# Kernel optimization log

Measured on AMD Instinct MI355X. Metric: run time of the kernel, lower is better.

The kernel has to match this reference:

```python
import jax, jax.numpy as jnp
import numpy as np
import math

B, D, TX, TY = 16, 192, 512, 2048
NEG = -1e9


def _neg_cent(x_mean, x_logs, z):
    # x_mean, x_logs: [B, D, TX]; z: [B, D, TY] -> neg_cent: [B, TY, TX]
    s_p_sq_r = jnp.exp(-2.0 * x_logs)                                   # [B,D,TX]
    nc1 = jnp.sum(-0.5 * math.log(2.0 * math.pi) - x_logs, axis=1, keepdims=True)  # [B,1,TX]
    nc2 = jnp.einsum('bdy,bdx->byx', -0.5 * z * z, s_p_sq_r)            # [B,TY,TX]
    nc3 = jnp.einsum('bdy,bdx->byx', z, x_mean * s_p_sq_r)              # [B,TY,TX]
    nc4 = jnp.sum(-0.5 * x_mean * x_mean * s_p_sq_r, axis=1, keepdims=True)  # [B,1,TX]
    return nc1 + nc2 + nc3 + nc4


def _mas_single(nc):
    # Monotonic alignment search (Viterbi DP) for one sample. nc: [TY, TX]
    ty, tx = nc.shape
    xs = jnp.arange(tx)

    def fwd_step(v_prev, inp):
        nc_row, y = inp
        v_diag = jnp.concatenate([jnp.full((1,), NEG, nc.dtype), v_prev[:-1]])
        take_diag = v_diag > v_prev                                      # bool [TX]
        v = nc_row + jnp.maximum(v_prev, v_diag)
        v = jnp.where(xs <= y, v, NEG)                                   # path cannot be ahead of time
        return v, take_diag

    v0 = jnp.where(xs == 0, nc[0], NEG)
    _, dirs = jax.lax.scan(fwd_step, v0, (nc[1:], jnp.arange(1, ty)))    # dirs: [TY-1, TX]

    def bwd_step(idx, d_row):
        # idx = path position at row y; move to y-1
        new_idx = idx - d_row[idx].astype(idx.dtype)
        return new_idx, idx

    idx0, path_tail = jax.lax.scan(bwd_step, jnp.array(tx - 1, jnp.int32), dirs, reverse=True)
    path = jnp.concatenate([idx0[None], path_tail])                      # [TY]
    return jax.nn.one_hot(path, tx, dtype=nc.dtype)                      # [TY, TX]


def _forward(x_mean, x_logs, z, logw):
    neg_cent = jax.lax.stop_gradient(_neg_cent(x_mean, x_logs, z))
    attn = jax.lax.stop_gradient(jax.vmap(_mas_single)(neg_cent))        # [B,TY,TX]
    w = jnp.sum(attn, axis=1, keepdims=True)                             # [B,1,TX] durations
    logw_ = jnp.log(w + 1e-6)
    l_length = jnp.sum((logw - logw_) ** 2, axis=(1, 2))                 # [B]
    m_p = jnp.einsum('byx,bdx->bdy', attn, x_mean)                       # [B,D,TY]
    logs_p = jnp.einsum('byx,bdx->bdy', attn, x_logs)                    # [B,D,TY]
    out_main = jnp.concatenate([m_p, logs_p], axis=1)                    # [B,2D,TY]
    return out_main, l_length, attn


def setup_inputs() -> dict:
    key = jax.random.key(0)
    k1, k2, k3, k4 = jax.random.split(key, 4)
    return {
        'x_mean': jax.random.normal(k1, (B, D, TX), jnp.float32),
        'x_logs': jax.random.normal(k2, (B, D, TX), jnp.float32),
        'z': jax.random.normal(k3, (B, D, TY), jnp.float32),
        'logw': jax.random.normal(k4, (B, 1, TX), jnp.float32),
    }


def reference(x_mean, x_logs, z, logw):
    return _forward(x_mean, x_logs, z, logw)
```

## Files before the change

kernel.cpp:

```cpp
#include <hip/hip_runtime.h>
#include <hip/hip_bf16.h>
#include <math.h>

#define B_   16
#define D_   192
#define TX_  512
#define TY_  2048
#define NEGV (-1e9f)



typedef __attribute__((address_space(1))) const float glob_f;
typedef __attribute__((address_space(3))) float       lds_f;

__global__ __launch_bounds__(512) void precomp(const float* __restrict__ xm,
                                               const float* __restrict__ xl,
                                               float* __restrict__ S,
                                               float* __restrict__ MS,
                                               float* __restrict__ Cpart) {
    int b = blockIdx.x;
    int p = blockIdx.y;
    int x = threadIdx.x;
    size_t base = ((size_t)b * D_ + p * 32) * TX_;
    const float* mb = xm + base;
    const float* lb = xl + base;
    float* Sb  = S  + base;
    float* MSb = MS + base;
    float c = 0.f;
    for (int d = 0; d < 32; d++) {
        float lg = lb[d * TX_ + x];
        float mn = mb[d * TX_ + x];
        float s  = expf(-2.f * lg);
        float ms = mn * s;
        Sb[d * TX_ + x]  = s;
        MSb[d * TX_ + x] = ms;
        c += -0.9189385332046727f - lg - 0.5f * mn * mn * s;
    }
    Cpart[(b * 6 + p) * TX_ + x] = c;
}

__global__ __launch_bounds__(256) void gemm_nc(const float* __restrict__ z,
                                               const float* __restrict__ S,
                                               const float* __restrict__ MS,
                                               const float* __restrict__ Cpart,
                                               float* __restrict__ NC) {
    int bx = blockIdx.x;
    int by = blockIdx.y;
    int b  = blockIdx.z;
    int tid = threadIdx.x;
    int tx = tid & 15, ty = tid >> 4;
    __shared__ __align__(16) float Zt[16 * 128];
    __shared__ __align__(16) float St[16 * 128];
    __shared__ __align__(16) float MSt[16 * 128];

    float acc[8][8];
#pragma unroll
    for (int i = 0; i < 8; i++)
#pragma unroll
        for (int j = 0; j < 8; j++) acc[i][j] = 0.f;

    int x0 = bx * 128, y0 = by * 128;
    const float* zb  = z  + (size_t)b * D_ * TY_;
    const float* Sb  = S  + (size_t)b * D_ * TX_;
    const float* MSb = MS + (size_t)b * D_ * TX_;

    for (int k0 = 0; k0 < D_; k0 += 16) {
#pragma unroll
        for (int j = 0; j < 2; j++) {
            int f = tid + j * 256;
            int kk = f >> 5, c = (f & 31) * 4;
            __builtin_amdgcn_global_load_lds((glob_f*)(zb  + (size_t)(k0 + kk) * TY_ + y0 + c),
                                             (lds_f*)(Zt  + f * 4), 16, 0, 0);
            __builtin_amdgcn_global_load_lds((glob_f*)(Sb  + (size_t)(k0 + kk) * TX_ + x0 + c),
                                             (lds_f*)(St  + f * 4), 16, 0, 0);
            __builtin_amdgcn_global_load_lds((glob_f*)(MSb + (size_t)(k0 + kk) * TX_ + x0 + c),
                                             (lds_f*)(MSt + f * 4), 16, 0, 0);
        }
        __syncthreads();

#pragma unroll 2
        for (int kk = 0; kk < 16; kk++) {
            float4 z0 = *(const float4*)&Zt[kk * 128 + ty * 4];
            float4 z1 = *(const float4*)&Zt[kk * 128 + 64 + ty * 4];
            float4 s0 = *(const float4*)&St[kk * 128 + tx * 4];
            float4 s1 = *(const float4*)&St[kk * 128 + 64 + tx * 4];
            float4 m0 = *(const float4*)&MSt[kk * 128 + tx * 4];
            float4 m1 = *(const float4*)&MSt[kk * 128 + 64 + tx * 4];
            float4 u0, u1;
            u0.x = -0.5f * z0.x * z0.x; u0.y = -0.5f * z0.y * z0.y;
            u0.z = -0.5f * z0.z * z0.z; u0.w = -0.5f * z0.w * z0.w;
            u1.x = -0.5f * z1.x * z1.x; u1.y = -0.5f * z1.y * z1.y;
            u1.z = -0.5f * z1.z * z1.z; u1.w = -0.5f * z1.w * z1.w;
            float zz[8] = {z0.x, z0.y, z0.z, z0.w, z1.x, z1.y, z1.z, z1.w};
            float uu[8] = {u0.x, u0.y, u0.z, u0.w, u1.x, u1.y, u1.z, u1.w};
            float ss[8] = {s0.x, s0.y, s0.z, s0.w, s1.x, s1.y, s1.z, s1.w};
            float mm[8] = {m0.x, m0.y, m0.z, m0.w, m1.x, m1.y, m1.z, m1.w};
#pragma unroll
            for (int i = 0; i < 8; i++)
#pragma unroll
                for (int j = 0; j < 8; j++)
                    acc[i][j] += uu[i] * ss[j] + zz[i] * mm[j];
        }
        __syncthreads();
    }

    float cv[8] = {0, 0, 0, 0, 0, 0, 0, 0};
#pragma unroll
    for (int p = 0; p < 6; p++) {
        float4 c0 = *(const float4*)&Cpart[(b * 6 + p) * TX_ + x0 + tx * 4];
        float4 c1 = *(const float4*)&Cpart[(b * 6 + p) * TX_ + x0 + 64 + tx * 4];
        cv[0] += c0.x; cv[1] += c0.y; cv[2] += c0.z; cv[3] += c0.w;
        cv[4] += c1.x; cv[5] += c1.y; cv[6] += c1.z; cv[7] += c1.w;
    }

#pragma unroll
    for (int i = 0; i < 8; i++) {
        int y = y0 + ty * 4 + (i & 3) + 64 * (i >> 2);
        float4 o0, o1;
        o0.x = acc[i][0] + cv[0]; o0.y = acc[i][1] + cv[1];
        o0.z = acc[i][2] + cv[2]; o0.w = acc[i][3] + cv[3];
        o1.x = acc[i][4] + cv[4]; o1.y = acc[i][5] + cv[5];
        o1.z = acc[i][6] + cv[6]; o1.w = acc[i][7] + cv[7];
        *(float4*)&NC[((size_t)b * TY_ + y) * TX_ + x0 + tx * 4]      = o0;
        *(float4*)&NC[((size_t)b * TY_ + y) * TX_ + x0 + 64 + tx * 4] = o1;
    }
}

__global__ __launch_bounds__(64, 1) void mas_forward(const float* __restrict__ NC,
                                                     unsigned char* __restrict__ dirs) {
    int b = blockIdx.x;
    int lane = threadIdx.x;
    const float* ncb = NC + (size_t)b * TY_ * TX_;
    const float4* base = (const float4*)ncb + lane * 2;

    float4 A[16], C[16];
#pragma unroll
    for (int s = 0; s < 16; s++) {
        A[s] = base[(size_t)(1 + s) * 128];
        C[s] = base[(size_t)(1 + s) * 128 + 1];
    }

    float v[8];
#pragma unroll
    for (int j = 0; j < 8; j++) v[j] = NEGV;
    if (lane == 0) v[0] = ncb[0];

    unsigned char* db = dirs + (size_t)b * 2048 * 64 + lane;

    float bound = NEGV;

    auto row_step = [&](float4 a, float4 c, int y, bool mask) {
        float ncv[8] = {a.x, a.y, a.z, a.w, c.x, c.y, c.z, c.w};
        float vd0 = (lane == 0) ? NEGV : bound;
        float v6o = v[6], v7o = v[7];
        float v7n = ncv[7] + fmaxf(v7o, v6o);
        if (mask && y < 511 && lane * 8 + 7 > y) v7n = NEGV;
        bound = __shfl_up(v7n, 1);
        unsigned bits = (v6o > v7o) ? 0x80u : 0u;
        float vd = vd0;
#pragma unroll
        for (int j = 0; j < 7; j++) {
            float vp = v[j];
            bits |= (vd > vp) ? (1u << j) : 0u;
            v[j] = ncv[j] + fmaxf(vp, vd);
            vd = vp;
        }
        if (mask && y < 511) {
            int xb = lane * 8;
#pragma unroll
            for (int j = 0; j < 7; j++)
                if (xb + j > y) v[j] = NEGV;
        }
        v[7] = v7n;
        db[(size_t)(y - 1) * 64] = (unsigned char)bits;
    };

    int y = 1;
    for (int k = 0; k < 32; k++) {
#pragma unroll
        for (int s = 0; s < 16; s++) {
            float4 a = A[s], c = C[s];
            A[s] = base[(size_t)(y + 16) * 128];
            C[s] = base[(size_t)(y + 16) * 128 + 1];
            row_step(a, c, y, true);
            y++;
        }
    }
    for (int k = 32; k < 127; k++) {
#pragma unroll
        for (int s = 0; s < 16; s++) {
            float4 a = A[s], c = C[s];
            A[s] = base[(size_t)(y + 16) * 128];
            C[s] = base[(size_t)(y + 16) * 128 + 1];
            row_step(a, c, y, false);
            y++;
        }
    }
#pragma unroll
    for (int s = 0; s < 15; s++) {
        row_step(A[s], C[s], y, false);
        y++;
    }
}

__global__ __launch_bounds__(64, 1) void mas_backtrack(const unsigned* __restrict__ dirs,
                                                       int* __restrict__ path) {
    int b = blockIdx.x;
    int lane = threadIdx.x;
    const unsigned* db = dirs + (size_t)b * 2048 * 16;
    int idx = TX_ - 1;

    for (int y_hi = 2047; y_hi >= 1; y_hi -= 64) {
        int wb = (idx >> 5) - 2;
        if (wb < 0) wb = 0;
        int base = wb << 5;
        int y = y_hi - lane;
        unsigned w0 = 0, w1 = 0, w2 = 0;
        if (y >= 1) {
            const unsigned* r = db + (size_t)(y - 1) * 16 + wb;
            w0 = r[0]; w1 = r[1]; w2 = r[2];
        }
        int steps = (y_hi < 64) ? y_hi : 64;
        int my_path = 0;
#pragma unroll 8
        for (int t = 0; t < steps; t++) {
            if (lane == t) my_path = idx;
            unsigned u0 = (unsigned)__shfl((int)w0, t);
            unsigned u1 = (unsigned)__shfl((int)w1, t);
            unsigned u2 = (unsigned)__shfl((int)w2, t);
            int off = idx - base;
            unsigned w = (off < 32) ? u0 : ((off < 64) ? u1 : u2);
            idx -= (int)((w >> (off & 31)) & 1u);
        }
        if (lane < steps) path[b * TY_ + (y_hi - lane)] = my_path;
    }
    if (lane == 0) path[b * TY_ + 0] = idx;
}

__global__ __launch_bounds__(512) void durations_ll(const int* __restrict__ path,
                                                    const float* __restrict__ logw,
                                                    float* __restrict__ out_l) {
    int b = blockIdx.x;
    int tid = threadIdx.x;
    __shared__ int wcnt[TX_];
    __shared__ float partial[8];
    wcnt[tid] = 0;
    __syncthreads();
    for (int y = tid; y < TY_; y += 512)
        atomicAdd(&wcnt[path[b * TY_ + y]], 1);
    __syncthreads();
    float t = logw[b * TX_ + tid] - logf((float)wcnt[tid] + 1e-6f);
    float sq = t * t;
#pragma unroll
    for (int off = 32; off > 0; off >>= 1) sq += __shfl_down(sq, off);
    if ((tid & 63) == 0) partial[tid >> 6] = sq;
    __syncthreads();
    if (tid == 0) {
        float s = 0.f;
#pragma unroll
        for (int i = 0; i < 8; i++) s += partial[i];
        out_l[b] = s;
    }
}

__global__ __launch_bounds__(256) void gather_main(const int* __restrict__ path,
                                                   const float* __restrict__ xm,
                                                   const float* __restrict__ xl,
                                                   float* __restrict__ out) {
    int c = blockIdx.x;
    int b = blockIdx.y;
    int tid = threadIdx.x;
    const float* src = (c < D_) ? (xm + ((size_t)b * D_ + c) * TX_)
                                : (xl + ((size_t)b * D_ + (c - D_)) * TX_);
    const int* pb = path + b * TY_;
    float* ob = out + ((size_t)b * 2 * D_ + c) * TY_;
#pragma unroll
    for (int k = 0; k < 8; k++) {
        int y = tid + k * 256;
        ob[y] = src[pb[y]];
    }
}

__global__ __launch_bounds__(128) void write_attn(const int* __restrict__ path,
                                                  float* __restrict__ attn) {
    int blk = blockIdx.x;
    int b = blk >> 11;
    int y = blk & 2047;
    int tid = threadIdx.x;
    int p = path[b * TY_ + y];
    float4 val = make_float4(0.f, 0.f, 0.f, 0.f);
    if ((p >> 2) == tid) {
        int r = p & 3;
        if (r == 0) val.x = 1.f;
        else if (r == 1) val.y = 1.f;
        else if (r == 2) val.z = 1.f;
        else val.w = 1.f;
    }
    ((float4*)attn)[((size_t)blk) * 128 + tid] = val;
}

extern "C" void kernel_launch(void* const* d_in, const int* in_sizes, int n_in,
                              void* d_out, int out_size, void* d_ws, size_t ws_size,
                              hipStream_t stream) {
    const float* x_mean = (const float*)d_in[0];
    const float* x_logs = (const float*)d_in[1];
    const float* z      = (const float*)d_in[2];
    const float* logw   = (const float*)d_in[3];
    float* out = (float*)d_out;

    char* ws = (char*)d_ws;
    float* S            = (float*)(ws + 0);
    float* MS           = (float*)(ws + 6291456);
    float* NC           = (float*)(ws + 12615680);
    unsigned char* dirs = (unsigned char*)(ws + 79724544);
    float* Cpart        = (float*)(ws + 79724544);
    int* path           = (int*)(ws + 81821696);

    float* out_main = out;
    float* out_l    = out + 12582912;
    float* out_attn = out + 12582928;

    precomp<<<dim3(B_, 6), dim3(512), 0, stream>>>(x_mean, x_logs, S, MS, Cpart);
    gemm_nc<<<dim3(4, 16, 16), dim3(256), 0, stream>>>(z, S, MS, Cpart, NC);
    mas_forward<<<dim3(B_), dim3(64), 0, stream>>>(NC, dirs);
    mas_backtrack<<<dim3(B_), dim3(64), 0, stream>>>((const unsigned*)dirs, path);
    durations_ll<<<dim3(B_), dim3(512), 0, stream>>>(path, logw, out_l);
    gather_main<<<dim3(384, 16), dim3(256), 0, stream>>>(path, x_mean, x_logs, out_main);
    write_attn<<<dim3(B_ * TY_), dim3(128), 0, stream>>>(path, out_attn);
}
```

Baseline: 752.3 us.

## Add producer wave streaming NC rows into LDS ring for MAS forward

The MAS forward kernel becomes a two-wave block: one producer wave copies chunks of 16 rows of neg_cent straight from global memory into a 4-slot LDS ring with global_load_lds, and the consumer wave runs the Viterbi recurrence from LDS. The two waves synchronise through workgroup-scope atomic counters with sleep-based spinning. This replaces the register-held 16-row prefetch, aiming to hide global load latency on the serial DP path. In exchange it adds 128KB of LDS, spin-wait overhead, and LDS read latency on every row.

```diff
diff --git a/kernel.cpp b/kernel.cpp
--- a/kernel.cpp
+++ b/kernel.cpp
@@ -126,80 +126,123 @@
     }
 }
 
-__global__ __launch_bounds__(64, 1) void mas_forward(const float* __restrict__ NC,
-                                                     unsigned char* __restrict__ dirs) {
+__global__ __launch_bounds__(128, 1) void mas_forward(const float* __restrict__ NC,
+                                                      unsigned char* __restrict__ dirs) {
     int b = blockIdx.x;
-    int lane = threadIdx.x;
+    int tid = threadIdx.x;
+    int wave = tid >> 6;
+    int lane = tid & 63;
     const float* ncb = NC + (size_t)b * TY_ * TX_;
-    const float4* base = (const float4*)ncb + lane * 2;
-
-    float4 A[16], C[16];
-#pragma unroll
-    for (int s = 0; s < 16; s++) {
-        A[s] = base[(size_t)(1 + s) * 128];
-        C[s] = base[(size_t)(1 + s) * 128 + 1];
-    }
-
-    float v[8];
-#pragma unroll
-    for (int j = 0; j < 8; j++) v[j] = NEGV;
-    if (lane == 0) v[0] = ncb[0];
-
-    unsigned char* db = dirs + (size_t)b * 2048 * 64 + lane;
-
-    float bound = NEGV;
-
-    auto row_step = [&](float4 a, float4 c, int y, bool mask) {
-        float ncv[8] = {a.x, a.y, a.z, a.w, c.x, c.y, c.z, c.w};
-        float vd0 = (lane == 0) ? NEGV : bound;
-        float v6o = v[6], v7o = v[7];
-        float v7n = ncv[7] + fmaxf(v7o, v6o);
-        if (mask && y < 511 && lane * 8 + 7 > y) v7n = NEGV;
-        bound = __shfl_up(v7n, 1);
-        unsigned bits = (v6o > v7o) ? 0x80u : 0u;
-        float vd = vd0;
-#pragma unroll
-        for (int j = 0; j < 7; j++) {
-            float vp = v[j];
-            bits |= (vd > vp) ? (1u << j) : 0u;
-            v[j] = ncv[j] + fmaxf(vp, vd);
-            vd = vp;
-        }
-        if (mask && y < 511) {
-            int xb = lane * 8;
-#pragma unroll
-            for (int j = 0; j < 7; j++)
-                if (xb + j > y) v[j] = NEGV;
-        }
-        v[7] = v7n;
-        db[(size_t)(y - 1) * 64] = (unsigned char)bits;
-    };
-
-    int y = 1;
-    for (int k = 0; k < 32; k++) {
-#pragma unroll
-        for (int s = 0; s < 16; s++) {
-            float4 a = A[s], c = C[s];
-            A[s] = base[(size_t)(y + 16) * 128];
-            C[s] = base[(size_t)(y + 16) * 128 + 1];
-            row_step(a, c, y, true);
-            y++;
-        }
-    }
-    for (int k = 32; k < 127; k++) {
-#pragma unroll
-        for (int s = 0; s < 16; s++) {
-            float4 a = A[s], c = C[s];
-            A[s] = base[(size_t)(y + 16) * 128];
-            C[s] = base[(size_t)(y + 16) * 128 + 1];
-            row_step(a, c, y, false);
-            y++;
-        }
-    }
-#pragma unroll
-    for (int s = 0; s < 15; s++) {
-        row_step(A[s], C[s], y, false);
-        y++;
+
+    __shared__ __align__(16) float ring[64][512];
+    __shared__ int prod_cnt;
+    __shared__ int cons_cnt;
+    if (tid == 0) { prod_cnt = 0; cons_cnt = 0; }
+    __syncthreads();
+
+    if (wave == 1) {
+        for (int k = 0; k < 128; k++) {
+            while (k - __hip_atomic_load(&cons_cnt, __ATOMIC_ACQUIRE,
+                                         __HIP_MEMORY_SCOPE_WORKGROUP) >= 4)
+                __builtin_amdgcn_s_sleep(1);
+            int slot0 = (k & 3) * 16;
+#pragma unroll
+            for (int r = 0; r < 16; r++) {
+                int y = 1 + k * 16 + r;
+                if (y > 2047) y = 2047;
+                const float* g = ncb + (size_t)y * TX_ + lane * 4;
+                float* l = &ring[slot0 + r][0];
+                __builtin_amdgcn_global_load_lds((glob_f*)g,         (lds_f*)l,         16, 0, 0);
+                __builtin_amdgcn_global_load_lds((glob_f*)(g + 256), (lds_f*)(l + 256), 16, 0, 0);
+            }
+            asm volatile("s_waitcnt vmcnt(0)" ::: "memory");
+            if (lane == 0)
+                __hip_atomic_store(&prod_cnt, k + 1, __ATOMIC_RELEASE,
+                                   __HIP_MEMORY_SCOPE_WORKGROUP);
+        }
+    } else {
+        float v[8];
+#pragma unroll
+        for (int j = 0; j < 8; j++) v[j] = NEGV;
+        if (lane == 0) v[0] = ncb[0];
+
+        unsigned char* db = dirs + (size_t)b * 2048 * 64 + lane;
+        float bound = NEGV;
+
+        auto row_step = [&](float4 a, float4 c, int y, bool mask) {
+            float ncv[8] = {a.x, a.y, a.z, a.w, c.x, c.y, c.z, c.w};
+            float vd0 = (lane == 0) ? NEGV : bound;
+            float v6o = v[6], v7o = v[7];
+            float v7n = ncv[7] + fmaxf(v7o, v6o);
+            if (mask && y < 511 && lane * 8 + 7 > y) v7n = NEGV;
+            bound = __shfl_up(v7n, 1);
+            unsigned bits = (v6o > v7o) ? 0x80u : 0u;
+            float vd = vd0;
+#pragma unroll
+            for (int j = 0; j < 7; j++) {
+                float vp = v[j];
+                bits |= (vd > vp) ? (1u << j) : 0u;
+                v[j] = ncv[j] + fmaxf(vp, vd);
+                vd = vp;
+            }
+            if (mask && y < 511) {
+                int xb = lane * 8;
+#pragma unroll
+                for (int j = 0; j < 7; j++)
+                    if (xb + j > y) v[j] = NEGV;
+            }
+            v[7] = v7n;
+            db[(size_t)(y - 1) * 64] = (unsigned char)bits;
+        };
+
+        auto wait_chunk = [&](int k) {
+            while (__hip_atomic_load(&prod_cnt, __ATOMIC_ACQUIRE,
+                                     __HIP_MEMORY_SCOPE_WORKGROUP) < k + 1)
+                __builtin_amdgcn_s_sleep(1);
+        };
+        auto done_chunk = [&](int k) {
+            if (lane == 0)
+                __hip_atomic_store(&cons_cnt, k + 1, __ATOMIC_RELEASE,
+                                   __HIP_MEMORY_SCOPE_WORKGROUP);
+        };
+
+        int y = 1;
+        for (int k = 0; k < 32; k++) {
+            wait_chunk(k);
+            int slot0 = (k & 3) * 16;
+#pragma unroll
+            for (int r = 0; r < 16; r++) {
+                float4 a = *(const float4*)&ring[slot0 + r][lane * 8];
+                float4 c = *(const float4*)&ring[slot0 + r][lane * 8 + 4];
+                row_step(a, c, y, true);
+                y++;
+            }
+            done_chunk(k);
+        }
+        for (int k = 32; k < 127; k++) {
+            wait_chunk(k);
+            int slot0 = (k & 3) * 16;
+#pragma unroll
+            for (int r = 0; r < 16; r++) {
+                float4 a = *(const float4*)&ring[slot0 + r][lane * 8];
+                float4 c = *(const float4*)&ring[slot0 + r][lane * 8 + 4];
+                row_step(a, c, y, false);
+                y++;
+            }
+            done_chunk(k);
+        }
+        wait_chunk(127);
+        {
+            int slot0 = (127 & 3) * 16;
+#pragma unroll
+            for (int r = 0; r < 15; r++) {
+                float4 a = *(const float4*)&ring[slot0 + r][lane * 8];
+                float4 c = *(const float4*)&ring[slot0 + r][lane * 8 + 4];
+                row_step(a, c, y, false);
+                y++;
+            }
+            done_chunk(127);
+        }
     }
 }
 
@@ -322,7 +365,7 @@
 
     precomp<<<dim3(B_, 6), dim3(512), 0, stream>>>(x_mean, x_logs, S, MS, Cpart);
     gemm_nc<<<dim3(4, 16, 16), dim3(256), 0, stream>>>(z, S, MS, Cpart, NC);
-    mas_forward<<<dim3(B_), dim3(64), 0, stream>>>(NC, dirs);
+    mas_forward<<<dim3(B_), dim3(128), 0, stream>>>(NC, dirs);
     mas_backtrack<<<dim3(B_), dim3(64), 0, stream>>>((const unsigned*)dirs, path);
     durations_ll<<<dim3(B_), dim3(512), 0, stream>>>(path, logw, out_l);
     gather_main<<<dim3(384, 16), dim3(256), 0, stream>>>(path, x_mean, x_logs, out_main);
```

New measurement: 799.1 us. 1.06x slower.
